# Optimization experiments

Hardware: AMD Instinct MI355X
Metric: run time of the kernel (lower is better)

Reference implementation:

```python
import jax, jax.numpy as jnp
import numpy as np

N, C, H, W = 16, 64, 128, 128
SHIFT = 1  # frozen value of torch module's random.randint(-2, 2) drawn at __init__


def setup_inputs() -> dict:
    key = jax.random.key(0)
    k1, k2, k3 = jax.random.split(key, 3)
    x = jax.random.normal(k1, (N, C, H, W), dtype=jnp.float32)
    # p_3: Conv2d(c, c, (1,5), padding=(0,2), bias=False) -> weight (C_out, C_in, 1, 5)
    w3 = jax.random.normal(k2, (C, C, 1, 5), dtype=jnp.float32) * (1.0 / np.sqrt(5.0 * C))
    # p_7: Conv2d(9c, c, 1, groups=c, bias=False) -> per output channel, 9 input channels: (C, 9)
    w7 = jax.random.normal(k3, (C, 9), dtype=jnp.float32) * (1.0 / 3.0)
    return {"x": x, "w3": w3, "w7": w7}


def reference(x, w3, w7):
    n, c, h, w = x.shape
    # t_1: F.unfold(x, (1,3), dilation=(1,2), padding=(0,2)) -> width offsets -2, 0, +2 (zero padded)
    xp = jnp.pad(x, ((0, 0), (0, 0), (0, 0), (2, 2)))
    t1 = jnp.stack([xp[..., 0:w], xp[..., 2:w + 2], xp[..., 4:w + 4]], axis=2)  # (n,c,3,h,w)
    # t_3: 1x5 conv, padding (0,2)
    t3 = jax.lax.conv_general_dilated(
        x, w3, window_strides=(1, 1), padding=[(0, 0), (2, 2)],
        dimension_numbers=("NCHW", "OIHW", "NCHW"))  # (n,c,h,w)
    # t_4: F.unfold(t1 as (n,3c,h,w), (3,1), padding=(1,0)) -> height offsets -1, 0, +1
    t1p = jnp.pad(t1, ((0, 0), (0, 0), (0, 0), (1, 1), (0, 0)))
    t4 = jnp.stack([t1p[..., 0:h, :], t1p[..., 1:h + 1, :], t1p[..., 2:h + 2, :]],
                   axis=3)  # (n, c, 3[w_off], 3[h_off], h, w)
    # t_5: roll along the W axis (dim 5)
    t5 = jnp.roll(t4, SHIFT, axis=5)
    # t_6: maximum of lhs (n,c,1,3,h,w) and rhs (n,c,3,3,h,w); lhs offset dim aligns with rhs dim 3
    t6 = jnp.maximum(t1[:, :, None, :, :, :], t5)  # (n,c,3,3,h,w)
    # t_7: grouped 1x1 conv, groups=c, 9 input channels per group -> 1 output channel
    t6f = t6.reshape(n, c, 9, h, w)
    t7 = jnp.einsum("nckhw,ck->nchw", t6f, w7)
    return t7 * t3
```

## Files before the change

### kernel.cpp

```cpp
#include <hip/hip_runtime.h>

#define NN 16
#define CC 64
#define HH 128
#define WW 128

#define LDS_STRIDE 72
#define PANEL_DW   4752
#define PANEL_SH   9504

typedef __attribute__((ext_vector_type(8))) short short8;
typedef __attribute__((ext_vector_type(4))) float floatx4;

__device__ __forceinline__ short f2bf(float f) {
    union { float f; unsigned u; } v; v.f = f;
    unsigned r = v.u + 0x7fffu + ((v.u >> 16) & 1u);
    return (short)(r >> 16);
}
__device__ __forceinline__ unsigned pack2bf(float lo, float hi) {
    union { float f; unsigned u; } a, b; a.f = lo; b.f = hi;
    unsigned ra = a.u + 0x7fffu + ((a.u >> 16) & 1u);
    unsigned rb = b.u + 0x7fffu + ((b.u >> 16) & 1u);
    return (ra >> 16) | (rb & 0xffff0000u);
}
__device__ __forceinline__ float bf2f(unsigned short u) {
    union { unsigned u; float f; } v; v.u = ((unsigned)u) << 16;
    return v.f;
}

__global__ __launch_bounds__(256) void prep_w(const float* __restrict__ w3,
                                              short* __restrict__ Abf,
                                              float* __restrict__ zp) {
    int idx = blockIdx.x * 256 + threadIdx.x;
    if (idx < CC * CC * 5) {
        int tap = idx % 5;
        int ci  = (idx / 5) % CC;
        int co  = idx / (5 * CC);
        Abf[co * 320 + tap * 64 + ci] = f2bf(w3[idx]);
    }
    if (blockIdx.x == 0 && threadIdx.x < 64) zp[threadIdx.x] = 0.f;
}

__global__ __launch_bounds__(256, 4) void t3gemm(const float* __restrict__ x,
                                                 const short* __restrict__ Abf,
                                                 float* __restrict__ out) {
    __shared__ __align__(16) char smem[2 * 19008];
    short*    xsT = (short*)smem;
    unsigned* xsW = (unsigned*)smem;

    const int bid = blockIdx.x;
    const int rp  = ((bid & 7) << 7) | (bid >> 3);
    const int n   = rp >> 6;
    const int h   = (rp & 63) * 2;
    const int tid = threadIdx.x;
    const int lane = tid & 63;
    const int W    = tid >> 6;

    {
        const int ri = lane >> 5;
        const int wq = lane & 31;
        unsigned* panel = xsW + ri * PANEL_DW;
        #pragma unroll
        for (int i = 0; i < 8; ++i) {
            const int cp = W * 8 + i;
            const float* b0 = x + (((size_t)(n * CC + 2 * cp)) * HH + h) * WW;
            float4 av = *(const float4*)(b0 + lane * 4);
            float4 bv = *(const float4*)(b0 + HH * WW + lane * 4);
            #pragma unroll
            for (int k = 0; k < 4; ++k) {
                int wp = wq * 4 + 2 + k;
                panel[wp * 36 + cp] = pack2bf(av[k], bv[k]);
            }
        }
        {
            int pi  = tid >> 7;
            int idx = tid & 127;
            int wpi = idx >> 5;
            int wpz = (wpi < 2) ? wpi : 128 + wpi;
            xsW[pi * PANEL_DW + wpz * 36 + (idx & 31)] = 0u;
        }
    }
    __syncthreads();

    const int lm = lane & 15;
    const int g  = lane >> 4;
    const int mh = W >> 1;
    const int wh = W & 1;

    const short* arow = Abf + (mh * 32 + lm) * 320;
    short* t3s = (short*)out;

    #pragma unroll
    for (int row = 0; row < 2; ++row) {
        const short* panel = xsT + row * PANEL_SH;

        floatx4 acc[2][4];
        #pragma unroll
        for (int m = 0; m < 2; ++m)
            #pragma unroll
            for (int j = 0; j < 4; ++j) acc[m][j] = (floatx4){0.f, 0.f, 0.f, 0.f};

        for (int ks = 0; ks < 10; ++ks) {
            const int kbase = ks * 32 + g * 8;
            const int tap   = kbase >> 6;
            const int cib   = kbase & 63;

            short8 a0 = *(const short8*)(arow + kbase);
            short8 a1 = *(const short8*)(arow + 16 * 320 + kbase);
            #pragma unroll
            for (int j = 0; j < 4; ++j) {
                int wp = (wh * 4 + j) * 16 + lm + tap;
                short8 b = *(const short8*)&panel[wp * LDS_STRIDE + cib];
                acc[0][j] = __builtin_amdgcn_mfma_f32_16x16x32_bf16(a0, b, acc[0][j], 0, 0, 0);
                acc[1][j] = __builtin_amdgcn_mfma_f32_16x16x32_bf16(a1, b, acc[1][j], 0, 0, 0);
            }
        }

        #pragma unroll
        for (int m = 0; m < 2; ++m)
            #pragma unroll
            for (int j = 0; j < 4; ++j)
                #pragma unroll
                for (int r = 0; r < 4; ++r) {
                    int co = (mh * 2 + m) * 16 + g * 4 + r;
                    int w  = (wh * 4 + j) * 16 + lm;
                    t3s[((size_t)(n * CC + co) * HH + (h + row)) * 256 + w] =
                        f2bf(acc[m][j][r]);
                }
    }
}

__global__ __launch_bounds__(256, 4) void combine(const float* __restrict__ x,
                                                  const float* __restrict__ w7,
                                                  const float* __restrict__ zp,
                                                  float* __restrict__ out) {
    const int bid = blockIdx.x;
    const int nh  = ((bid & 7) << 8) | (bid >> 3);
    const int n   = nh >> 7;
    const int h   = nh & (HH - 1);
    const int tid = threadIdx.x;
    const int lane = tid & 63;

    const int w0  = (tid & 31) * 4;
    const int chi = tid >> 5;
    const bool isw = (w0 == 0);
    const int src  = lane | 31;

    const float* p[9];
    int s[9];
    const float* xb0 = x + (((size_t)(n * CC + chi)) * HH) * WW;
    #pragma unroll
    for (int r = 0; r < 3; ++r) {
        int hh = h + r - 1;
        bool hok = (unsigned)hh < HH;
        #pragma unroll
        for (int q = 0; q < 3; ++q) {
            int cb = w0 - 4 + q * 4;
            bool ok = hok && (unsigned)cb < WW;
            p[r * 3 + q] = ok ? (xb0 + (size_t)hh * WW + cb) : zp;
            s[r * 3 + q] = ok ? (8 * HH * WW) : 0;
        }
    }
    const float* wcp = w7 + chi * 9;
    const short* t3s = (const short*)out;
    size_t t3o = ((size_t)(n * CC + chi) * HH + h) * 256 + w0;
    float* outp = out + ((((size_t)(n * CC + chi)) * HH + h) * WW) + w0;

    #pragma unroll
    for (int it = 0; it < 8; ++it) {
        float4 cur[9];
        #pragma unroll
        for (int t = 0; t < 9; ++t) { cur[t] = *(const float4*)p[t]; p[t] += s[t]; }
        float wc[9];
        #pragma unroll
        for (int t = 0; t < 9; ++t) wc[t] = wcp[t];
        ushort4 tv = *(const ushort4*)&t3s[t3o];

        float win[3][12];
        #pragma unroll
        for (int r = 0; r < 3; ++r) {
            #pragma unroll
            for (int q = 0; q < 3; ++q) {
                float4 v = cur[r * 3 + q];
                win[r][q * 4 + 0] = v.x; win[r][q * 4 + 1] = v.y;
                win[r][q * 4 + 2] = v.z; win[r][q * 4 + 3] = v.w;
            }
        }
        float wrap0[3], wrap1[3];
        #pragma unroll
        for (int r = 0; r < 3; ++r) {
            wrap0[r] = __shfl(win[r][5], src);
            wrap1[r] = __shfl(win[r][7], src);
        }

        float t3v[4] = {bf2f(tv.x), bf2f(tv.y), bf2f(tv.z), bf2f(tv.w)};

        float res[4];
        #pragma unroll
        for (int e = 0; e < 4; ++e) {
            float a = 0.f;
            #pragma unroll
            for (int j = 0; j < 3; ++j) {
                #pragma unroll
                for (int i = 0; i < 3; ++i) {
                    float lhs = win[1][e + 2 * i + 2];
                    float rhs = win[i][e + 2 * j + 1];
                    if (e == 0)
                        rhs = isw ? ((j == 0) ? wrap0[i]
                                   : (j == 1) ? wrap1[i] : 0.f)
                                  : rhs;
                    a = fmaf(wc[j * 3 + i], fmaxf(lhs, rhs), a);
                }
            }
            res[e] = a;
        }
        float4 o;
        o.x = res[0] * t3v[0]; o.y = res[1] * t3v[1];
        o.z = res[2] * t3v[2]; o.w = res[3] * t3v[3];
        *(float4*)outp = o;

        wcp  += 8 * 9;
        t3o  += (size_t)8 * HH * 256;
        outp += (size_t)8 * HH * WW;
    }
}

extern "C" void kernel_launch(void* const* d_in, const int* in_sizes, int n_in,
                              void* d_out, int out_size, void* d_ws, size_t ws_size,
                              hipStream_t stream) {
    const float* x  = (const float*)d_in[0];
    const float* w3 = (const float*)d_in[1];
    const float* w7 = (const float*)d_in[2];
    float* out = (float*)d_out;

    short* Abf = (short*)d_ws;
    float* zp  = (float*)((char*)d_ws + 40960);

    prep_w<<<(CC * CC * 5 + 255) / 256, 256, 0, stream>>>(w3, Abf, zp);
    t3gemm<<<NN * HH / 2, 256, 0, stream>>>(x, Abf, out);
    combine<<<NN * HH, 256, 0, stream>>>(x, w7, zp, out);
}
```

Measured before the change: 162.0 us.

## Split transpose into separate kernel and stream panels via global_load_lds in GEMM

The fused transpose+GEMM kernel is split in two. A new transp kernel writes bf16 channel-interleaved row panels to workspace. The GEMM kernel then loads one row's panel directly into LDS with global_load_lds, uses one row per block with higher occupancy, and reads weights pre-packed into the MFMA fragment layout for coalesced loads. The aim is to remove the in-GEMM fp32 load and transpose latency and improve occupancy, at the cost of an extra kernel launch and an extra round-trip of the bf16 panels through global memory.

After: 168.5 us. 4.0% more time.

```diff
diff --git a/kernel.cpp b/kernel.cpp
--- a/kernel.cpp
+++ b/kernel.cpp
@@ -7,7 +7,8 @@
 
 #define LDS_STRIDE 72
 #define PANEL_DW   4752
-#define PANEL_SH   9504
+#define ROW_BYTES  19008
+#define ROW_CHUNKS 1188
 
 typedef __attribute__((ext_vector_type(8))) short short8;
 typedef __attribute__((ext_vector_type(4))) float floatx4;
@@ -27,25 +28,31 @@
     union { unsigned u; float f; } v; v.u = ((unsigned)u) << 16;
     return v.f;
 }
+__device__ __forceinline__ void gload_lds16(const void* g, void* l) {
+    __builtin_amdgcn_global_load_lds(
+        (const __attribute__((address_space(1))) void*)g,
+        (__attribute__((address_space(3))) void*)l, 16, 0, 0);
+}
 
 __global__ __launch_bounds__(256) void prep_w(const float* __restrict__ w3,
-                                              short* __restrict__ Abf,
+                                              short* __restrict__ Apk,
                                               float* __restrict__ zp) {
     int idx = blockIdx.x * 256 + threadIdx.x;
-    if (idx < CC * CC * 5) {
-        int tap = idx % 5;
-        int ci  = (idx / 5) % CC;
-        int co  = idx / (5 * CC);
-        Abf[co * 320 + tap * 64 + ci] = f2bf(w3[idx]);
+    if (idx < CC * 320) {
+        int co = idx / 320;
+        int kk = idx % 320;
+        int mh = co >> 5, m = (co >> 4) & 1, lm = co & 15;
+        int ks = kk >> 5, g = (kk >> 3) & 3, e = kk & 7;
+        int tap = kk >> 6, ci = kk & 63;
+        Apk[((((mh * 10 + ks) * 2 + m) * 64) + (g * 16 + lm)) * 8 + e] =
+            f2bf(w3[(co * CC + ci) * 5 + tap]);
     }
     if (blockIdx.x == 0 && threadIdx.x < 64) zp[threadIdx.x] = 0.f;
 }
 
-__global__ __launch_bounds__(256, 4) void t3gemm(const float* __restrict__ x,
-                                                 const short* __restrict__ Abf,
-                                                 float* __restrict__ out) {
-    __shared__ __align__(16) char smem[2 * 19008];
-    short*    xsT = (short*)smem;
+__global__ __launch_bounds__(256, 4) void transp(const float* __restrict__ x,
+                                                 short* __restrict__ xT) {
+    __shared__ __align__(16) char smem[2 * ROW_BYTES];
     unsigned* xsW = (unsigned*)smem;
 
     const int bid = blockIdx.x;
@@ -82,52 +89,86 @@
     }
     __syncthreads();
 
+    const size_t rowb = (size_t)(n * HH + h) * ROW_BYTES;
+    #pragma unroll
+    for (int pi = 0; pi < 2; ++pi) {
+        short8* dst = (short8*)((char*)xT + rowb + (size_t)pi * ROW_BYTES);
+        const short8* src = (const short8*)(smem + pi * ROW_BYTES);
+        #pragma unroll
+        for (int i = 0; i < 5; ++i) {
+            int c = tid + 256 * i;
+            if (c < ROW_CHUNKS) dst[c] = src[c];
+        }
+    }
+}
+
+__global__ __launch_bounds__(256, 8) void t3gemm(const short* __restrict__ xT,
+                                                 const short* __restrict__ Apk,
+                                                 float* __restrict__ out) {
+    __shared__ __align__(16) char smem[19456];
+    const short* panel = (const short*)smem;
+
+    const int bid = blockIdx.x;
+    const int nh  = ((bid & 7) << 8) | (bid >> 3);
+    const int n   = nh >> 7;
+    const int h   = nh & (HH - 1);
+    const int tid = threadIdx.x;
+    const int lane = tid & 63;
+    const int W    = tid >> 6;
+
+    {
+        const char* grow = (const char*)xT + (size_t)(n * HH + h) * ROW_BYTES;
+        #pragma unroll
+        for (int k2 = 0; k2 < 5; ++k2) {
+            int base = (k2 * 4 + W) * 1024;
+            if (base < ROW_BYTES) {
+                int goff = base + lane * 16;
+                if (goff > ROW_BYTES - 16) goff = ROW_BYTES - 16;
+                gload_lds16(grow + goff, smem + base);
+            }
+        }
+    }
+    __syncthreads();
+
     const int lm = lane & 15;
     const int g  = lane >> 4;
     const int mh = W >> 1;
     const int wh = W & 1;
 
-    const short* arow = Abf + (mh * 32 + lm) * 320;
+    floatx4 acc[2][4];
+    #pragma unroll
+    for (int m = 0; m < 2; ++m)
+        #pragma unroll
+        for (int j = 0; j < 4; ++j) acc[m][j] = (floatx4){0.f, 0.f, 0.f, 0.f};
+
+    for (int ks = 0; ks < 10; ++ks) {
+        const int kbase = ks * 32 + g * 8;
+        const int tap   = kbase >> 6;
+        const int cib   = kbase & 63;
+
+        const short* ab = Apk + (((mh * 10 + ks) * 2) * 64 + lane) * 8;
+        short8 a0 = *(const short8*)ab;
+        short8 a1 = *(const short8*)(ab + 64 * 8);
+        #pragma unroll
+        for (int j = 0; j < 4; ++j) {
+            int wp = (wh * 4 + j) * 16 + lm + tap;
+            short8 b = *(const short8*)&panel[wp * LDS_STRIDE + cib];
+            acc[0][j] = __builtin_amdgcn_mfma_f32_16x16x32_bf16(a0, b, acc[0][j], 0, 0, 0);
+            acc[1][j] = __builtin_amdgcn_mfma_f32_16x16x32_bf16(a1, b, acc[1][j], 0, 0, 0);
+        }
+    }
+
     short* t3s = (short*)out;
-
-    #pragma unroll
-    for (int row = 0; row < 2; ++row) {
-        const short* panel = xsT + row * PANEL_SH;
-
-        floatx4 acc[2][4];
-        #pragma unroll
-        for (int m = 0; m < 2; ++m)
-            #pragma unroll
-            for (int j = 0; j < 4; ++j) acc[m][j] = (floatx4){0.f, 0.f, 0.f, 0.f};
-
-        for (int ks = 0; ks < 10; ++ks) {
-            const int kbase = ks * 32 + g * 8;
-            const int tap   = kbase >> 6;
-            const int cib   = kbase & 63;
-
-            short8 a0 = *(const short8*)(arow + kbase);
-            short8 a1 = *(const short8*)(arow + 16 * 320 + kbase);
-            #pragma unroll
-            for (int j = 0; j < 4; ++j) {
-                int wp = (wh * 4 + j) * 16 + lm + tap;
-                short8 b = *(const short8*)&panel[wp * LDS_STRIDE + cib];
-                acc[0][j] = __builtin_amdgcn_mfma_f32_16x16x32_bf16(a0, b, acc[0][j], 0, 0, 0);
-                acc[1][j] = __builtin_amdgcn_mfma_f32_16x16x32_bf16(a1, b, acc[1][j], 0, 0, 0);
-            }
-        }
-
-        #pragma unroll
-        for (int m = 0; m < 2; ++m)
-            #pragma unroll
-            for (int j = 0; j < 4; ++j)
-                #pragma unroll
-                for (int r = 0; r < 4; ++r) {
-                    int co = (mh * 2 + m) * 16 + g * 4 + r;
-                    int w  = (wh * 4 + j) * 16 + lm;
-                    t3s[((size_t)(n * CC + co) * HH + (h + row)) * 256 + w] =
-                        f2bf(acc[m][j][r]);
-                }
-    }
+    #pragma unroll
+    for (int m = 0; m < 2; ++m)
+        #pragma unroll
+        for (int j = 0; j < 4; ++j)
+            #pragma unroll
+            for (int r = 0; r < 4; ++r) {
+                int co = (mh * 2 + m) * 16 + g * 4 + r;
+                int w  = (wh * 4 + j) * 16 + lm;
+                t3s[((size_t)(n * CC + co) * HH + h) * 256 + w] = f2bf(acc[m][j][r]);
+            }
 }
 
 __global__ __launch_bounds__(256, 4) void combine(const float* __restrict__ x,
@@ -233,10 +274,12 @@
     const float* w7 = (const float*)d_in[2];
     float* out = (float*)d_out;
 
-    short* Abf = (short*)d_ws;
+    short* Apk = (short*)d_ws;
     float* zp  = (float*)((char*)d_ws + 40960);
-
-    prep_w<<<(CC * CC * 5 + 255) / 256, 256, 0, stream>>>(w3, Abf, zp);
-    t3gemm<<<NN * HH / 2, 256, 0, stream>>>(x, Abf, out);
+    short* xT  = (short*)((char*)d_ws + 65536);
+
+    prep_w<<<(CC * 320 + 255) / 256, 256, 0, stream>>>(w3, Apk, zp);
+    transp<<<NN * HH / 2, 256, 0, stream>>>(x, xT);
+    t3gemm<<<NN * HH, 256, 0, stream>>>(xT, Apk, out);
     combine<<<NN * HH, 256, 0, stream>>>(x, w7, zp, out);
 }
```
